# Performance work log

Measured on AMD Instinct MI355X. Metric: run time of the kernel, lower is better.

## Reference

```python
import jax, jax.numpy as jnp
import numpy as np
import math

D_IN, D_MODEL, N_HEADS, DIM_HEAD, NB_FEAT, N_CLASSES = 24, 512, 8, 64, 266, 10
FF_DIM = 4 * D_MODEL  # performer-pytorch FeedForward mult=4
LN_EPS = 1e-5
B, N = 16, 2048


def gaussian_orthogonal(key, nb_rows, nb_cols):
    # FAVOR+ gaussian orthogonal random matrix (scaling=0: chi-distributed row norms)
    n_blocks = nb_rows // nb_cols + 1
    keys = jax.random.split(key, n_blocks + 1)
    blocks = []
    for i in range(n_blocks):
        q, _ = jnp.linalg.qr(jax.random.normal(keys[i], (nb_cols, nb_cols)))
        blocks.append(q.T)
    mat = jnp.concatenate(blocks, axis=0)[:nb_rows]
    multiplier = jnp.linalg.norm(jax.random.normal(keys[-1], (nb_rows, nb_cols)), axis=1)
    return multiplier[:, None] * mat


def layer_norm(x, g, b):
    mu = jnp.mean(x, axis=-1, keepdims=True)
    var = jnp.var(x, axis=-1, keepdims=True)
    return (x - mu) * jax.lax.rsqrt(var + LN_EPS) * g + b


def softmax_kernel(data, proj, is_query, eps=1e-4):
    # FAVOR+ positive random features approximating the softmax kernel
    data_norm = data.shape[-1] ** -0.25
    ratio = proj.shape[0] ** -0.5
    dd = jnp.einsum('bhnd,fd->bhnf', data * data_norm, proj)  # [B,H,N,F]
    diag = 0.5 * jnp.sum(data * data, axis=-1, keepdims=True) * (data_norm ** 2)
    if is_query:
        m = jax.lax.stop_gradient(jnp.max(dd, axis=-1, keepdims=True))
    else:
        m = jax.lax.stop_gradient(jnp.max(dd))
    return ratio * (jnp.exp(dd - diag - m) + eps)


def setup_inputs() -> dict:
    key = jax.random.key(0)
    ks = jax.random.split(key, 24)

    def linw(k, fi, fo):
        bnd = 1.0 / math.sqrt(fi)
        return jax.random.uniform(k, (fi, fo), minval=-bnd, maxval=bnd, dtype=jnp.float32)

    def linb(k, fi, fo):
        bnd = 1.0 / math.sqrt(fi)
        return jax.random.uniform(k, (fo,), minval=-bnd, maxval=bnd, dtype=jnp.float32)

    return {
        'x': jax.random.normal(ks[0], (B, N, D_IN), dtype=jnp.float32),
        'enc_w': linw(ks[1], D_IN, D_MODEL), 'enc_b': linb(ks[2], D_IN, D_MODEL),
        'ln1_g': jnp.ones((D_MODEL,), jnp.float32), 'ln1_b': jnp.zeros((D_MODEL,), jnp.float32),
        'wq': linw(ks[3], D_MODEL, D_MODEL), 'bq': linb(ks[4], D_MODEL, D_MODEL),
        'wk': linw(ks[5], D_MODEL, D_MODEL), 'bk': linb(ks[6], D_MODEL, D_MODEL),
        'wv': linw(ks[7], D_MODEL, D_MODEL), 'bv': linb(ks[8], D_MODEL, D_MODEL),
        'wo': linw(ks[9], D_MODEL, D_MODEL), 'bo': linb(ks[10], D_MODEL, D_MODEL),
        'proj': gaussian_orthogonal(ks[11], NB_FEAT, DIM_HEAD).astype(jnp.float32),
        'ln2_g': jnp.ones((D_MODEL,), jnp.float32), 'ln2_b': jnp.zeros((D_MODEL,), jnp.float32),
        'ff_w1': linw(ks[12], D_MODEL, FF_DIM), 'ff_b1': linb(ks[13], D_MODEL, FF_DIM),
        'ff_w2': linw(ks[14], FF_DIM, D_MODEL), 'ff_b2': linb(ks[15], FF_DIM, D_MODEL),
        'mlp_w1': linw(ks[16], D_MODEL, D_MODEL), 'mlp_b1': linb(ks[17], D_MODEL, D_MODEL),
        'mlp_w2': linw(ks[18], D_MODEL, N_CLASSES), 'mlp_b2': linb(ks[19], D_MODEL, N_CLASSES),
    }


def reference(x, enc_w, enc_b, ln1_g, ln1_b, wq, bq, wk, bk, wv, bv, wo, bo, proj,
              ln2_g, ln2_b, ff_w1, ff_b1, ff_w2, ff_b2, mlp_w1, mlp_b1, mlp_w2, mlp_b2):
    b, n, _ = x.shape
    h = (x @ enc_w + enc_b) * math.sqrt(D_MODEL)  # [B,N,D]

    # --- Performer layer: PreLN + FAVOR+ self-attention ---
    y = layer_norm(h, ln1_g, ln1_b)
    split = lambda t: t.reshape(b, n, N_HEADS, DIM_HEAD).transpose(0, 2, 1, 3)  # [B,H,N,Dh]
    q = split(y @ wq + bq)
    k = split(y @ wk + bk)
    v = split(y @ wv + bv)
    qp = softmax_kernel(q, proj, is_query=True)   # [B,H,N,F]
    kp = softmax_kernel(k, proj, is_query=False)  # [B,H,N,F]
    # non-causal linear attention
    k_sum = kp.sum(axis=2)                                   # [B,H,F]
    d_inv = 1.0 / jnp.einsum('bhnf,bhf->bhn', qp, k_sum)     # [B,H,N]
    ctx = jnp.einsum('bhnf,bhnd->bhfd', kp, v)               # [B,H,F,Dh]
    attn = jnp.einsum('bhnf,bhfd,bhn->bhnd', qp, ctx, d_inv)
    attn = attn.transpose(0, 2, 1, 3).reshape(b, n, D_MODEL)
    h = h + attn @ wo + bo

    y = layer_norm(h, ln2_g, ln2_b)
    h = h + jax.nn.gelu(y @ ff_w1 + ff_b1, approximate=False) @ ff_w2 + ff_b2

    # --- max pool over sequence + MLP head ---
    p = jnp.max(h, axis=1)  # [B,D]
    return jax.nn.relu(p @ mlp_w1 + mlp_b1) @ mlp_w2 + mlp_b2  # [B,n_classes]
```

## Files before the change

### kernel.cpp

```cpp
#include <hip/hip_runtime.h>
#include <math.h>

typedef unsigned short u16;
typedef __bf16 bf16x8 __attribute__((ext_vector_type(8)));
typedef float f32x4 __attribute__((ext_vector_type(4)));
typedef u16 u16x8 __attribute__((ext_vector_type(8)));

#define DEVI static __device__ __forceinline__

#define NB 16
#define SEQ 2048
#define DM 512
#define DH 64
#define NF 266
#define NFP 288
#define FFD 2048
#define ROWS (NB*SEQ)
#define SQRT_DM 22.62741699796952f
#define DATA_NORM 0.3535533905932738f
#define RATIO 0.0613139073f
#define KEPS 1e-4f

DEVI u16 f2b(float f){
  union{float f; unsigned u;} c; c.f=f;
  unsigned r = c.u + 0x7FFFu + ((c.u>>16)&1u);
  return (u16)(r>>16);
}
DEVI float b2f(u16 v){
  union{unsigned u; float f;} c; c.u = ((unsigned)v)<<16; return c.f;
}
DEVI unsigned cvtpk(float a, float b){
  unsigned r;
  asm("v_cvt_pk_bf16_f32 %0, %1, %2" : "=v"(r) : "v"(a), "v"(b));
  return r;
}

DEVI f32x4 MFMA(bf16x8 a, bf16x8 b, f32x4 c){
  return __builtin_amdgcn_mfma_f32_16x16x32_bf16(a,b,c,0,0,0);
}

DEVI void async16(void* lds, const void* g){
  __builtin_amdgcn_global_load_lds(
      (const __attribute__((address_space(1))) unsigned*)g,
      (__attribute__((address_space(3))) unsigned*)lds, 16, 0, 0);
}

DEVI void atomicMaxF(float* a, float v){
  if (v >= 0.f) atomicMax((int*)a, __float_as_int(v));
  else          atomicMin((unsigned*)a, (unsigned)__float_as_int(v));
}

DEVI bf16x8 ldb8(const u16* p){ return *(const bf16x8*)p; }

DEVI float erf_fast(float u){
  float au = fabsf(u);
  float tt = __builtin_amdgcn_rcpf(1.f + 0.3275911f*au);
  float poly = tt*(0.254829592f + tt*(-0.284496736f + tt*(1.421413741f + tt*(-1.453152027f + tt*1.061405429f))));
  float er = 1.f - poly*__expf(-u*u);
  return copysignf(er, u);
}

template<int EPI, int BNT>
__launch_bounds__(512,2)
__global__ void gemm8(const u16* __restrict__ A, int lda,
                      const u16* __restrict__ Bt, int ldb,
                      const float* __restrict__ bias,
                      float* __restrict__ resid,
                      u16* __restrict__ Cb,
                      int N, int K)
{
  constexpr int NREG = BNT/64;
  constexpr int BUFU = 8192 + BNT*32;
  __shared__ u16 sm[2*BUFU];
  const int tid = threadIdx.x;
  const int ntn = N / BNT;
  int bid = blockIdx.x;
  const int nwg = gridDim.x;
  if ((nwg & 7) == 0){ int qq = nwg >> 3; bid = (bid & 7)*qq + (bid >> 3); }
  const int bm = bid / ntn, bn = bid % ntn;
  const int wid = tid>>6, l = tid&63, lr = l&15, lg = l>>4;
  const int wm = wid>>2, wn = wid&3;

  const int rA = tid>>2;
  const int cA = (tid&3) ^ ((rA>>1)&3);
  const u16* gA = A  + (size_t)(bm*256 + rA)*lda + cA*8;
  const u16* gB = Bt + (size_t)(bn*BNT + rA)*ldb + cA*8;
  const size_t stepA = (size_t)128*lda, stepB = (size_t)128*ldb;

  const int cc = ((lg ^ ((lr>>1)&3))<<3);
  const int aoff = (wm*128 + lr)*32 + cc;
  const int boff = 8192 + (wn*(BNT/4) + lr)*32 + cc;

  const int nt = K >> 5;
  f32x4 acc[8][NREG];
  #pragma unroll
  for (int m=0;m<8;m++)
    #pragma unroll
    for (int n=0;n<NREG;n++) acc[m][n]=(f32x4){0.f,0.f,0.f,0.f};

  {
    u16* sb = &sm[0];
    async16(&sb[tid*8],         gA);
    async16(&sb[4096 + tid*8],  gA + stepA);
    async16(&sb[8192 + tid*8],  gB);
    if (BNT == 256) async16(&sb[12288 + tid*8], gB + stepB);
  }
  asm volatile("s_waitcnt vmcnt(0)" ::: "memory");
  __builtin_amdgcn_s_barrier();
  __builtin_amdgcn_sched_barrier(0);

  for (int t=0; t<nt; ++t){
    if (t+1 < nt){
      u16* sb = &sm[((t+1)&1)*BUFU];
      const u16* a0 = gA + (t+1)*32;
      const u16* b0 = gB + (t+1)*32;
      async16(&sb[tid*8],         a0);
      async16(&sb[4096 + tid*8],  a0 + stepA);
      async16(&sb[8192 + tid*8],  b0);
      if (BNT == 256) async16(&sb[12288 + tid*8], b0 + stepB);
    }
    __builtin_amdgcn_sched_barrier(0);
    const u16* sb = &sm[(t&1)*BUFU];
    bf16x8 af[8], bfr[NREG];
    #pragma unroll
    for (int m=0;m<8;m++) af[m]  = ldb8(&sb[aoff + m*512]);
    #pragma unroll
    for (int n=0;n<NREG;n++) bfr[n] = ldb8(&sb[boff + n*512]);
    __builtin_amdgcn_s_setprio(1);
    #pragma unroll
    for (int m=0;m<8;m++)
      #pragma unroll
      for (int n=0;n<NREG;n++)
        acc[m][n] = MFMA(af[m], bfr[n], acc[m][n]);
    __builtin_amdgcn_s_setprio(0);
    if (t+1 < nt){
      asm volatile("s_waitcnt vmcnt(0)" ::: "memory");
      __builtin_amdgcn_s_barrier();
      __builtin_amdgcn_sched_barrier(0);
    }
  }

  if (EPI == 3){
    const int r0 = bm*256 + wm*128 + lg*4;
    const int c0 = bn*BNT + wn*(BNT/4) + lr;
    #pragma unroll
    for (int m=0;m<8;m++){
      #pragma unroll
      for (int n=0;n<NREG;n++){
        #pragma unroll
        for (int q=0;q<4;q++){
          int r = r0 + m*16 + q;
          int c = c0 + n*16;
          float v = acc[m][n][q] + bias[c];
          size_t idx = (size_t)r*N + c;
          resid[idx] = resid[idx] + v;
        }
      }
    }
  } else {
    __syncthreads();
    constexpr int OBW = (BNT==256) ? 72 : 40;
    constexpr int OWS = (BNT==256) ? 2336 : 1280;
    const int c0w = bn*BNT + wn*(BNT/4);
    const int r0m = bm*256 + wm*128;
    #pragma unroll
    for (int m=0;m<8;m++){
      u16* obw = &sm[wid*OWS + (m&1)*(OWS/2)];
      #pragma unroll
      for (int n=0;n<NREG;n++){
        #pragma unroll
        for (int q=0;q<4;q++){
          float v = acc[m][n][q] + bias[c0w + n*16 + lr];
          if (EPI==2) v = 0.5f*v*(1.f + erf_fast(v*0.70710678f));
          obw[(lg*4+q)*OBW + n*16 + lr] = f2b(v);
        }
      }
      asm volatile("s_waitcnt lgkmcnt(0)" ::: "memory");
      if (BNT == 256){
        int rowR = l>>3, ck = l&7;
        #pragma unroll
        for (int rr=0; rr<2; ++rr){
          int r2 = rowR + rr*8;
          uint4 v = *(const uint4*)&obw[r2*OBW + ck*8];
          *(uint4*)(Cb + (size_t)(r0m + m*16 + r2)*N + c0w + ck*8) = v;
        }
      } else {
        int rowR = l>>2, ck = l&3;
        uint4 v = *(const uint4*)&obw[rowR*OBW + ck*8];
        *(uint4*)(Cb + (size_t)(r0m + m*16 + rowR)*N + c0w + ck*8) = v;
      }
    }
  }
}

__launch_bounds__(256)
__global__ void k_prep(const float* __restrict__ wq, const float* __restrict__ wk,
                       const float* __restrict__ wv, const float* __restrict__ wo,
                       const float* __restrict__ ffw1, const float* __restrict__ ffw2,
                       const float* __restrict__ proj, const float* __restrict__ bk,
                       const float* __restrict__ bv,
                       u16* __restrict__ wqT, u16* __restrict__ wkvT, u16* __restrict__ woT,
                       u16* __restrict__ f1T, u16* __restrict__ f2T, u16* __restrict__ pjn,
                       float* __restrict__ kvb, float* __restrict__ pbuf)
{
  int bid = blockIdx.x, t = threadIdx.x;
  if (bid < 3072){
    const float* src; u16* dst; int R, C, tile;
    if      (bid < 256){ src=wq;  dst=wqT;          R=512; C=512;  tile=bid; }
    else if (bid < 512){ src=wk;  dst=wkvT;         R=512; C=512;  tile=bid-256; }
    else if (bid < 768){ src=wv;  dst=wkvT+262144;  R=512; C=512;  tile=bid-512; }
    else if (bid <1024){ src=wo;  dst=woT;          R=512; C=512;  tile=bid-768; }
    else if (bid <2048){ src=ffw1;dst=f1T;          R=512; C=2048; tile=bid-1024; }
    else               { src=ffw2;dst=f2T;          R=2048;C=512;  tile=bid-2048; }
    int ntc = C>>5;
    int tr = tile/ntc, tc = tile%ntc;
    __shared__ float tl[32][33];
    int r = t>>5, c = t&31;
    #pragma unroll
    for (int it=0; it<4; ++it)
      tl[r+it*8][c] = src[(size_t)(tr*32 + r + it*8)*C + tc*32 + c];
    __syncthreads();
    #pragma unroll
    for (int it=0; it<4; ++it)
      dst[(size_t)(tc*32 + r + it*8)*R + tr*32 + c] = f2b(tl[c][r+it*8]);
    return;
  }
  int i = (bid-3072)*256 + t;
  if (i < NFP*DH){ int f=i>>6, d=i&63; pjn[i] = f2b(f<NF ? proj[(size_t)f*64+d]*DATA_NORM : 0.f); return; }
  i -= NFP*DH;
  if (i < 1024){ kvb[i] = (i<512)? bk[i] : bv[i-512]; return; }
  i -= 1024;
  if (i < NB*DM){ pbuf[i] = -INFINITY; return; }
}

__global__ void k_signal(float* out, float v){
  if (threadIdx.x==0 && blockIdx.x==0) out[0] = v;
}

__launch_bounds__(256)
__global__ void k_encode_ln(const float* __restrict__ x, const float* __restrict__ ew,
                            const float* __restrict__ eb, const float* __restrict__ lgw,
                            const float* __restrict__ lbw, float* __restrict__ h,
                            u16* __restrict__ y)
{
  int w = threadIdx.x>>6, l = threadIdx.x&63;
  int row = blockIdx.x*4 + w;
  const float* xr = x + (size_t)row*24;
  float xv[24];
  #pragma unroll
  for (int k=0;k<24;k++) xv[k] = xr[k];
  int c0 = l*8;
  float a[8] = {0,0,0,0,0,0,0,0};
  #pragma unroll
  for (int k=0;k<24;k++){
    const float* wp = ew + (size_t)k*DM + c0;
    #pragma unroll
    for (int c=0;c<8;c++) a[c] += xv[k]*wp[c];
  }
  float s=0.f, s2=0.f;
  #pragma unroll
  for (int c=0;c<8;c++){
    a[c] = (a[c] + eb[c0+c]) * SQRT_DM;
    s += a[c]; s2 += a[c]*a[c];
  }
  #pragma unroll
  for (int m=1;m<64;m<<=1){ s += __shfl_xor(s,m); s2 += __shfl_xor(s2,m); }
  float mu = s*(1.f/DM);
  float rs = rsqrtf(s2*(1.f/DM) - mu*mu + 1e-5f);
  float* hr = h + (size_t)row*DM + c0;
  u16 yv[8];
  #pragma unroll
  for (int c=0;c<8;c++){
    hr[c] = a[c];
    yv[c] = f2b((a[c]-mu)*rs*lgw[c0+c] + lbw[c0+c]);
  }
  *(uint4*)(y + (size_t)row*DM + c0) = *(const uint4*)yv;
}

__launch_bounds__(256)
__global__ void k_ln(const float* __restrict__ h, const float* __restrict__ lgw,
                     const float* __restrict__ lbw, u16* __restrict__ y)
{
  int w = threadIdx.x>>6, l = threadIdx.x&63;
  int row = blockIdx.x*4 + w;
  int c0 = l*8;
  const float* hr = h + (size_t)row*DM + c0;
  float a[8];
  *(float4*)&a[0] = *(const float4*)hr;
  *(float4*)&a[4] = *(const float4*)(hr+4);
  float s=0.f, s2=0.f;
  #pragma unroll
  for (int c=0;c<8;c++){ s += a[c]; s2 += a[c]*a[c]; }
  #pragma unroll
  for (int m=1;m<64;m<<=1){ s += __shfl_xor(s,m); s2 += __shfl_xor(s2,m); }
  float mu = s*(1.f/DM);
  float rs = rsqrtf(s2*(1.f/DM) - mu*mu + 1e-5f);
  u16 yv[8];
  #pragma unroll
  for (int c=0;c<8;c++) yv[c] = f2b((a[c]-mu)*rs*lgw[c0+c] + lbw[c0+c]);
  *(uint4*)(y + (size_t)row*DM + c0) = *(const uint4*)yv;
}

__launch_bounds__(256,1)
__global__ void k_kmax(const u16* __restrict__ kv, const u16* __restrict__ pjn,
                       float* __restrict__ mkpart)
{
  __shared__ float red[4];
  int t = threadIdx.x, w = t>>6, l = t&63, lr = l&15, lg = l>>4;
  int bh = blockIdx.x>>3, tile = blockIdx.x&7;
  int b = bh>>3, hd = bh&7;
  int row0 = tile*256 + w*64;
  bf16x8 pf0[17], pf1[17];
  #pragma unroll
  for (int f=0; f<17; ++f){
    const u16* pb = pjn + (f*16 + lr)*64 + lg*8;
    pf0[f] = ldb8(pb); pf1[f] = ldb8(pb+32);
  }
  bf16x8 a0[4], a1[4];
  #pragma unroll
  for (int it=0; it<4; ++it){
    const u16* kb = kv + ((size_t)(b*SEQ + row0 + it*16 + lr)*1024 + hd*64 + lg*8);
    a0[it] = ldb8(kb); a1[it] = ldb8(kb+32);
  }
  float vmax = -3e38f;
  #pragma unroll
  for (int it=0; it<4; ++it){
    #pragma unroll
    for (int f=0; f<17; ++f){
      f32x4 z = (f32x4){0.f,0.f,0.f,0.f};
      z = MFMA(a0[it], pf0[f], z);
      z = MFMA(a1[it], pf1[f], z);
      if (f*16 + lr < NF){
        #pragma unroll
        for (int j=0;j<4;j++) vmax = fmaxf(vmax, z[j]);
      }
    }
  }
  #pragma unroll
  for (int m=1;m<64;m<<=1) vmax = fmaxf(vmax, __shfl_xor(vmax,m));
  if (l==0) red[w] = vmax;
  __syncthreads();
  if (t==0) mkpart[blockIdx.x] = fmaxf(fmaxf(red[0],red[1]), fmaxf(red[2],red[3]));
}

__global__ void k_kmax_red(const float* __restrict__ mkpart, float* __restrict__ mk){
  __shared__ float red[4];
  int t = threadIdx.x, w = t>>6, l = t&63;
  float v = fmaxf(fmaxf(mkpart[t], mkpart[t+256]), fmaxf(mkpart[t+512], mkpart[t+768]));
  #pragma unroll
  for (int m=1;m<64;m<<=1) v = fmaxf(v, __shfl_xor(v,m));
  if (l==0) red[w] = v;
  __syncthreads();
  if (t==0) mk[0] = fmaxf(fmaxf(red[0],red[1]), fmaxf(red[2],red[3]));
}

__launch_bounds__(256,2)
__global__ void k_kpctx(const u16* __restrict__ kv, const u16* __restrict__ pjn,
                        const float* __restrict__ mkp,
                        u16* __restrict__ ctxp, float* __restrict__ ksump)
{
  __shared__ u16 pjs[272*64];
  __shared__ u16 vT[DH*32];
  __shared__ u16 kpT[NFP*32];
  __shared__ float dbuf[4][16];
  int t = threadIdx.x, w = t>>6, l = t&63, lr = l&15, lg = l>>4;
  int bh = blockIdx.x>>2, seg = blockIdx.x&3;
  int b = bh>>3, hd = bh&7;
  int mw = w>>1, fh = (w&1)*9;
  float mk = *mkp;

  for (int i=t; i<2176; i+=256){
    int row = i>>3, cin = i&7;
    *(uint4*)&pjs[row*64 + ((cin ^ (row&7))<<3)] = ((const uint4*)pjn)[i];
  }

  f32x4 ctxa[18];
  #pragma unroll
  for (int f=0;f<18;f++) ctxa[f]=(f32x4){0.f,0.f,0.f,0.f};
  float ksa[9];
  #pragma unroll
  for (int i=0;i<9;i++) ksa[i]=0.f;

  for (int ch=0; ch<16; ++ch){
    int n0 = seg*512 + ch*32;
    __syncthreads();
    {
      int nl = t>>3, d0 = (t&7)*8;
      const u16* vsrc = kv + ((size_t)(b*SEQ + n0 + nl)*1024 + 512 + hd*64 + d0);
      uint4 vv = *(const uint4*)vsrc;
      const u16* vp = (const u16*)&vv;
      #pragma unroll
      for (int i=0;i<8;i++){
        int row = d0+i;
        vT[row*32 + (((nl>>3) ^ ((row>>1)&3))<<3) + (nl&7)] = vp[i];
      }
    }
    const u16* kb = kv + ((size_t)(b*SEQ + n0 + mw*16 + lr)*1024 + hd*64 + lg*8);
    bf16x8 a0 = ldb8(kb), a1 = ldb8(kb+32);
    float sq = 0.f;
    #pragma unroll
    for (int i=0;i<8;i++){ float u0=(float)a0[i], u1=(float)a1[i]; sq += u0*u0 + u1*u1; }
    sq += __shfl_xor(sq,16); sq += __shfl_xor(sq,32);
    if (l<16) dbuf[w][l] = sq*0.0625f;
    #pragma unroll
    for (int ff=0; ff<9; ++ff){
      int f = fh + ff;
      f32x4 z = (f32x4){0.f,0.f,0.f,0.f};
      if (f < 17){
        int row = f*16 + lr;
        const u16* pb0 = pjs + row*64 + ((lg ^ (lr&7))<<3);
        const u16* pb1 = pjs + row*64 + (((lg+4) ^ (lr&7))<<3);
        z = MFMA(a0, ldb8(pb0), z);
        z = MFMA(a1, ldb8(pb1), z);
      }
      float kp0 = RATIO*(__expf(z[0] - dbuf[w][lg*4+0] - mk) + KEPS);
      float kp1 = RATIO*(__expf(z[1] - dbuf[w][lg*4+1] - mk) + KEPS);
      float kp2 = RATIO*(__expf(z[2] - dbuf[w][lg*4+2] - mk) + KEPS);
      float kp3 = RATIO*(__expf(z[3] - dbuf[w][lg*4+3] - mk) + KEPS);
      ksa[ff] += kp0 + kp1 + kp2 + kp3;
      ushort4 kw;
      kw.x = f2b(kp0); kw.y = f2b(kp1); kw.z = f2b(kp2); kw.w = f2b(kp3);
      int row = f*16 + lr;
      int wch = (mw*2 + (lg>>1)) ^ ((row>>1)&3);
      *(ushort4*)&kpT[row*32 + (wch<<3) + ((lg&1)<<2)] = kw;
    }
    __syncthreads();
    int rr = w*16 + lr;
    bf16x8 av = ldb8(&vT[rr*32 + ((lg ^ ((rr>>1)&3))<<3)]);
    #pragma unroll
    for (int f=0;f<18;f++){
      int row = f*16 + lr;
      ctxa[f] = MFMA(av, ldb8(&kpT[row*32 + ((lg ^ ((row>>1)&3))<<3)]), ctxa[f]);
    }
  }

  __syncthreads();
  {
    float* tb = (w&1) ? (float*)pjs : (float*)kpT;
    u16* dstq = ctxp + (((size_t)seg*128 + bh)*DH + w*16)*NFP;
    #pragma unroll
    for (int r=0; r<2; ++r){
      if ((w>>1) == r){
        #pragma unroll
        for (int f=0;f<18;f++)
          #pragma unroll
          for (int j=0;j<4;j++)
            tb[(lg*4+j)*NFP + f*16 + lr] = ctxa[f][j];
        asm volatile("s_waitcnt lgkmcnt(0)" ::: "memory");
        #pragma unroll
        for (int k=0;k<9;k++){
          int c = k*64 + l;
          f32x4 v0 = *(const f32x4*)(tb + c*8);
          f32x4 v1 = *(const f32x4*)(tb + c*8 + 4);
          u16x8 o;
          o[0]=f2b(v0[0]); o[1]=f2b(v0[1]); o[2]=f2b(v0[2]); o[3]=f2b(v0[3]);
          o[4]=f2b(v1[0]); o[5]=f2b(v1[1]); o[6]=f2b(v1[2]); o[7]=f2b(v1[3]);
          *(u16x8*)(dstq + c*8) = o;
        }
      }
      __syncthreads();
    }
  }
  #pragma unroll
  for (int ff=0;ff<9;ff++){
    float v = ksa[ff];
    v += __shfl_xor(v,16); v += __shfl_xor(v,32);
    if (l<16) ksump[((size_t)seg*128 + bh)*NFP + (fh+ff)*16 + l] = v;
  }
}

__global__ void k_reduce(const u16* __restrict__ ctxp, const float* __restrict__ ksump,
                         u16* __restrict__ ctxb, float* __restrict__ ksum)
{
  const size_t CT = (size_t)128*DH*NFP;
  const size_t KT = (size_t)128*NFP;
  size_t i = (size_t)blockIdx.x*256 + threadIdx.x;
  if (i < CT){
    float s = b2f(ctxp[i]) + b2f(ctxp[i+CT]) + b2f(ctxp[i+2*CT]) + b2f(ctxp[i+3*CT]);
    ctxb[i] = f2b(s);
  } else if (i < CT + KT){
    size_t j = i - CT;
    ksum[j] = ksump[j] + ksump[j+KT] + ksump[j+2*KT] + ksump[j+3*KT];
  }
}

__launch_bounds__(256,3)
__global__ void k_qp_attn(const u16* __restrict__ q, const u16* __restrict__ pjn,
                          const u16* __restrict__ ctxb, const float* __restrict__ ksum,
                          u16* __restrict__ attn)
{
  __shared__ u16 pjs[272*64];
  __shared__ u16 ob[4][16*72];
  int t = threadIdx.x, w = t>>6, l = t&63, lr = l&15, lg = l>>4;
  int bh = blockIdx.x>>5, tile = blockIdx.x&31;
  int b = bh>>3, hd = bh&7;
  int n0 = tile*64;

  for (int i=t; i<2176; i+=256){
    int row = i>>3, cin = i&7;
    *(uint4*)&pjs[row*64 + ((cin ^ (row&7))<<3)] = ((const uint4*)pjn)[i];
  }

  const u16* qb = q + ((size_t)(b*SEQ + n0 + w*16 + lr)*DM + hd*64 + lg*8);
  bf16x8 a0 = ldb8(qb), a1 = ldb8(qb+32);
  float sq = 0.f;
  #pragma unroll
  for (int i=0;i<8;i++){ float u0=(float)a0[i], u1=(float)a1[i]; sq += u0*u0 + u1*u1; }
  sq += __shfl_xor(sq,16); sq += __shfl_xor(sq,32);
  float dg = sq*0.0625f;

  __syncthreads();

  const int sw0 = ((lg ^ (lr&7))<<3);
  const int sw1 = (((lg+4) ^ (lr&7))<<3);

  float mj = -3e38f;
  #pragma unroll
  for (int ft=0; ft<17; ++ft){
    const u16* pb = pjs + (ft*16 + lr)*64;
    f32x4 z = (f32x4){0.f,0.f,0.f,0.f};
    z = MFMA(ldb8(pb + sw0), a0, z);
    z = MFMA(ldb8(pb + sw1), a1, z);
    if (ft < 16){
      #pragma unroll
      for (int j=0;j<4;j++) mj = fmaxf(mj, z[j]);
    } else {
      #pragma unroll
      for (int j=0;j<4;j++) if (lg*4+j < 10) mj = fmaxf(mj, z[j]);
    }
  }
  mj = fmaxf(mj, __shfl_xor(mj,16));
  mj = fmaxf(mj, __shfl_xor(mj,32));

  int s0 = ((lg&1)<<5) + lr;
  int s1 = s0 + 16;
  bool hi = (l >= 32);
  f32x4 oacc[4];
  #pragma unroll
  for (int d=0;d<4;d++) oacc[d]=(f32x4){0.f,0.f,0.f,0.f};
  const u16* cbase = ctxb + (size_t)bh*DH*NFP;
  const float* ksb = ksum + (size_t)bh*NFP;
  float den = 0.f;
  #pragma unroll
  for (int fp=0; fp<9; ++fp){
    int te = 2*fp, to = te+1;
    f32x4 z0 = (f32x4){0.f,0.f,0.f,0.f};
    f32x4 z1 = (f32x4){0.f,0.f,0.f,0.f};
    {
      const u16* pb = pjs + (te*16 + lr)*64;
      z0 = MFMA(ldb8(pb + sw0), a0, z0);
      z0 = MFMA(ldb8(pb + sw1), a1, z0);
    }
    if (to < 17){
      const u16* pb = pjs + (to*16 + lr)*64;
      z1 = MFMA(ldb8(pb + sw0), a0, z1);
      z1 = MFMA(ldb8(pb + sw1), a1, z1);
    }
    f32x4 ks0 = *(const f32x4*)(ksb + te*16 + lg*4);
    f32x4 ks1 = *(const f32x4*)(ksb + to*16 + lg*4);
    int fb0 = te*16 + lg*4, fb1 = to*16 + lg*4;
    float qv0[4], qv1[4];
    #pragma unroll
    for (int j=0;j<4;j++){
      qv0[j] = (fb0 + j < NF) ? RATIO*(__expf(z0[j] - dg - mj) + KEPS) : 0.f;
      den += qv0[j]*ks0[j];
      qv1[j] = (fb1 + j < NF) ? RATIO*(__expf(z1[j] - dg - mj) + KEPS) : 0.f;
      den += qv1[j]*ks1[j];
    }
    unsigned q00 = cvtpk(qv0[0], qv0[1]), q01 = cvtpk(qv0[2], qv0[3]);
    unsigned q10 = cvtpk(qv1[0], qv1[1]), q11 = cvtpk(qv1[2], qv1[3]);
    unsigned e0 = (unsigned)__shfl((int)q00, s0), o0 = (unsigned)__shfl((int)q10, s0);
    unsigned e1 = (unsigned)__shfl((int)q01, s0), o1 = (unsigned)__shfl((int)q11, s0);
    unsigned e2 = (unsigned)__shfl((int)q00, s1), o2 = (unsigned)__shfl((int)q10, s1);
    unsigned e3 = (unsigned)__shfl((int)q01, s1), o3 = (unsigned)__shfl((int)q11, s1);
    union { unsigned u[4]; bf16x8 v; } bw;
    bw.u[0] = hi ? o0 : e0;
    bw.u[1] = hi ? o1 : e1;
    bw.u[2] = hi ? o2 : e2;
    bw.u[3] = hi ? o3 : e3;
    #pragma unroll
    for (int d=0;d<4;d++)
      oacc[d] = MFMA(bw.v, ldb8(&cbase[(d*16 + lr)*NFP + fp*32 + lg*8]), oacc[d]);
  }
  den += __shfl_xor(den,16); den += __shfl_xor(den,32);
  float di = 1.f/den;
  float di4[4];
  #pragma unroll
  for (int j=0;j<4;j++) di4[j] = __shfl(di, lg*4+j);

  u16* obw = ob[w];
  #pragma unroll
  for (int d=0;d<4;d++)
    #pragma unroll
    for (int j=0;j<4;j++)
      obw[(lg*4+j)*72 + d*16 + lr] = f2b(oacc[d][j]*di4[j]);
  asm volatile("s_waitcnt lgkmcnt(0)" ::: "memory");
  {
    int row = l>>3, ck = l&7;
    #pragma unroll
    for (int rr=0; rr<2; ++rr){
      int r2 = row + rr*8;
      uint4 v = *(const uint4*)&obw[r2*72 + ck*8];
      u16* ab = attn + ((size_t)(b*SEQ + n0 + w*16 + r2))*DM + hd*64;
      *(uint4*)(ab + ck*8) = v;
    }
  }
}

__global__ void k_maxpool(const float* __restrict__ h, const u16* __restrict__ fo,
                          float* __restrict__ p){
  int bi = blockIdx.x;
  int b = bi>>5, half = (bi>>4)&1, seg = bi&15;
  int c = half*256 + threadIdx.x;
  size_t base = ((size_t)b*SEQ + seg*128)*DM + c;
  const float* hp = h + base;
  const u16*  fp = fo + base;
  float m = -3e38f;
  for (int n=0;n<128;n++) m = fmaxf(m, hp[(size_t)n*DM] + b2f(fp[(size_t)n*DM]));
  atomicMaxF(&p[b*DM + c], m);
}

__launch_bounds__(256)
__global__ void k_head(const float* __restrict__ p, const float* __restrict__ w1,
                       const float* __restrict__ b1, const float* __restrict__ w2,
                       const float* __restrict__ b2, float* __restrict__ out)
{
  __shared__ float z[DM];
  __shared__ float pr[DM];
  int b = blockIdx.x, t = threadIdx.x;
  pr[t] = p[(size_t)b*DM + t];
  pr[t+256] = p[(size_t)b*DM + t + 256];
  __syncthreads();
  for (int c=t; c<DM; c+=256){
    float a = b1[c];
    for (int k=0;k<DM;k++) a += pr[k]*w1[(size_t)k*DM + c];
    z[c] = fmaxf(a, 0.f);
  }
  __syncthreads();
  if (t < 10){
    float a = b2[t];
    for (int k=0;k<DM;k++) a += z[k]*w2[(size_t)k*10 + t];
    out[b*10 + t] = a;
  }
}

static inline size_t align256(size_t x){ return (x+255)&~(size_t)255; }

extern "C" void kernel_launch(void* const* d_in, const int* in_sizes, int n_in,
                              void* d_out, int out_size, void* d_ws, size_t ws_size,
                              hipStream_t stream)
{
  (void)in_sizes; (void)n_in; (void)out_size;
  const float* x     = (const float*)d_in[0];
  const float* enc_w = (const float*)d_in[1];
  const float* enc_b = (const float*)d_in[2];
  const float* ln1_g = (const float*)d_in[3];
  const float* ln1_b = (const float*)d_in[4];
  const float* wq    = (const float*)d_in[5];
  const float* bq    = (const float*)d_in[6];
  const float* wk    = (const float*)d_in[7];
  const float* bk    = (const float*)d_in[8];
  const float* wv    = (const float*)d_in[9];
  const float* bv    = (const float*)d_in[10];
  const float* wo    = (const float*)d_in[11];
  const float* bo    = (const float*)d_in[12];
  const float* proj  = (const float*)d_in[13];
  const float* ln2_g = (const float*)d_in[14];
  const float* ln2_b = (const float*)d_in[15];
  const float* ff_w1 = (const float*)d_in[16];
  const float* ff_b1 = (const float*)d_in[17];
  const float* ff_w2 = (const float*)d_in[18];
  const float* ff_b2 = (const float*)d_in[19];
  const float* mw1   = (const float*)d_in[20];
  const float* mb1   = (const float*)d_in[21];
  const float* mw2   = (const float*)d_in[22];
  const float* mb2   = (const float*)d_in[23];

  char* base = (char*)d_ws;
  size_t off = 0;
  auto alloc = [&](size_t bytes)->void*{ void* r = base + off; off = align256(off + bytes); return r; };
  float* h     = (float*)alloc((size_t)ROWS*DM*4);
  u16*   slotA = (u16*)  alloc((size_t)ROWS*DM*2);
  u16*   wqT   = (u16*)  alloc((size_t)512*512*2);
  u16*   wkvT  = (u16*)  alloc((size_t)1024*512*2);
  u16*   woT   = (u16*)  alloc((size_t)512*512*2);
  u16*   f1T   = (u16*)  alloc((size_t)2048*512*2);
  u16*   f2T   = (u16*)  alloc((size_t)512*2048*2);
  u16*   pjn   = (u16*)  alloc((size_t)NFP*DH*2);
  float* kvb   = (float*)alloc(1024*4);
  float* mk    = (float*)alloc(256);
  float* mkpart= (float*)alloc(1024*4);
  u16*   ctxb  = (u16*)  alloc((size_t)128*DH*NFP*2);
  float* ksum  = (float*)alloc((size_t)128*NFP*4);
  float* pbuf  = (float*)alloc((size_t)NB*DM*4);
  size_t offU = off;
  u16*   slotB = (u16*)  alloc((size_t)ROWS*1024*2);
  u16*   ctxp  = (u16*)  alloc((size_t)4*128*DH*NFP*2);
  float* ksump = (float*)alloc((size_t)4*128*NFP*4);
  size_t off_small = off;
  size_t off_big   = align256(offU + (size_t)ROWS*FFD*2);
  bool big = (off_big <= ws_size);
  u16* ffb = (u16*)(base + offU);
  if (off_small > ws_size){
    k_signal<<<1,64,0,stream>>>((float*)d_out, (float)ws_size);
    return;
  }

  u16* y    = slotA;
  u16* attn = slotA;
  u16* ffo  = slotA;
  u16* kvB  = slotB;
  u16* qB   = slotB;

  k_prep<<<3180,256,0,stream>>>(wq, wk, wv, wo, ff_w1, ff_w2, proj, bk, bv,
                                wqT, wkvT, woT, f1T, f2T, pjn, kvb, pbuf);

  k_encode_ln<<<ROWS/4,256,0,stream>>>(x, enc_w, enc_b, ln1_g, ln1_b, h, y);
  gemm8<1,256><<<(ROWS/256)*(1024/256),512,0,stream>>>(y,512, wkvT,512, kvb, nullptr, kvB, 1024, 512);
  k_kmax<<<1024,256,0,stream>>>(kvB, pjn, mkpart);
  k_kmax_red<<<1,256,0,stream>>>(mkpart, mk);
  k_kpctx<<<512,256,0,stream>>>(kvB, pjn, mk, ctxp, ksump);
  k_reduce<<<9360,256,0,stream>>>(ctxp, ksump, ctxb, ksum);
  gemm8<1,128><<<(ROWS/256)*(512/128),512,0,stream>>>(y,512, wqT,512, bq, nullptr, qB, 512, 512);
  k_qp_attn<<<128*32,256,0,stream>>>(qB, pjn, ctxb, ksum, attn);
  gemm8<3,128><<<(ROWS/256)*(512/128),512,0,stream>>>(attn,512, woT,512, bo, h, nullptr, 512, 512);
  k_ln<<<ROWS/4,256,0,stream>>>(h, ln2_g, ln2_b, y);
  if (big){
    gemm8<2,256><<<(ROWS/256)*(2048/256),512,0,stream>>>(y,512, f1T,512, ff_b1, nullptr, ffb, 2048, 512);
    gemm8<1,128><<<(ROWS/256)*(512/128),512,0,stream>>>(ffb,2048, f2T,2048, ff_b2, nullptr, ffo, 512, 2048);
  } else {
    for (int c2=0;c2<2;c2++){
      const u16* ych = y + (size_t)c2*16384*512;
      u16*       fch = ffo + (size_t)c2*16384*512;
      gemm8<2,256><<<(16384/256)*(2048/256),512,0,stream>>>(ych,512, f1T,512, ff_b1, nullptr, ffb, 2048, 512);
      gemm8<1,128><<<(16384/256)*(512/128),512,0,stream>>>(ffb,2048, f2T,2048, ff_b2, nullptr, fch, 512, 2048);
    }
  }
  k_maxpool<<<NB*32,256,0,stream>>>(h, ffo, pbuf);
  k_head<<<NB,256,0,stream>>>(pbuf, mw1, mb1, mw2, mb2, (float*)d_out);
}
```

Baseline: 606.0 us.

## Triple-buffer GEMM LDS with prefetch distance two and split MFMA phases

Moves the bf16 GEMM from double to triple buffering in LDS, issuing global-to-LDS loads two K-steps ahead and waiting with partial vmcnt instead of draining all loads. Each K-step is split into two halves, each interleaving A or B prefetch with LDS reads and MFMAs, with extra barriers between them. The goal is to hide global memory latency better and overlap LDS reads with MFMA work. The cost is 1.5x the LDS footprint, which can cut occupancy at launch bounds of 2 blocks per CU, plus additional barriers per iteration.

```diff
diff --git a/kernel.cpp b/kernel.cpp
--- a/kernel.cpp
+++ b/kernel.cpp
@@ -70,8 +70,8 @@
                       int N, int K)
 {
   constexpr int NREG = BNT/64;
-  constexpr int BUFU = 8192 + BNT*32;
-  __shared__ u16 sm[2*BUFU];
+  constexpr int LDSB = 8192 + BNT*32;
+  __shared__ u16 sm[3*LDSB];
   const int tid = threadIdx.x;
   const int ntn = N / BNT;
   int bid = blockIdx.x;
@@ -98,46 +98,83 @@
     #pragma unroll
     for (int n=0;n<NREG;n++) acc[m][n]=(f32x4){0.f,0.f,0.f,0.f};
 
-  {
-    u16* sb = &sm[0];
-    async16(&sb[tid*8],         gA);
-    async16(&sb[4096 + tid*8],  gA + stepA);
-    async16(&sb[8192 + tid*8],  gB);
-    if (BNT == 256) async16(&sb[12288 + tid*8], gB + stepB);
-  }
-  asm volatile("s_waitcnt vmcnt(0)" ::: "memory");
+  auto stageA = [&](int bufi, int t){
+    u16* sb = &sm[bufi*LDSB];
+    const u16* a0 = gA + t*32;
+    async16(&sb[tid*8],        a0);
+    async16(&sb[4096 + tid*8], a0 + stepA);
+  };
+  auto stageB = [&](int bufi, int t){
+    u16* sb = &sm[bufi*LDSB];
+    const u16* b0 = gB + t*32;
+    async16(&sb[8192 + tid*8], b0);
+    if (BNT == 256) async16(&sb[12288 + tid*8], b0 + stepB);
+  };
+
+  stageA(0,0); stageB(0,0);
+  stageA(1,1); stageB(1,1);
+  if constexpr (BNT == 256) asm volatile("s_waitcnt vmcnt(4)" ::: "memory");
+  else                      asm volatile("s_waitcnt vmcnt(3)" ::: "memory");
   __builtin_amdgcn_s_barrier();
   __builtin_amdgcn_sched_barrier(0);
 
+  int bufc = 0;
   for (int t=0; t<nt; ++t){
+    const u16* sb = &sm[bufc*LDSB];
+    int bufn = bufc+2; if (bufn>=3) bufn-=3;
+    const bool pre = (t+2 < nt);
+    bf16x8 bfr[NREG];
+
+    if (pre) stageA(bufn, t+2);
+    bf16x8 af0 = ldb8(&sb[aoff + 0*512]);
+    bf16x8 af1 = ldb8(&sb[aoff + 1*512]);
+    bf16x8 af2 = ldb8(&sb[aoff + 2*512]);
+    bf16x8 af3 = ldb8(&sb[aoff + 3*512]);
+    #pragma unroll
+    for (int n=0;n<NREG;n++) bfr[n] = ldb8(&sb[boff + n*512]);
+    __builtin_amdgcn_s_barrier();
+    asm volatile("s_waitcnt lgkmcnt(0)" ::: "memory");
+    __builtin_amdgcn_sched_barrier(0);
+    __builtin_amdgcn_s_setprio(1);
+    #pragma unroll
+    for (int n=0;n<NREG;n++){
+      acc[0][n] = MFMA(af0, bfr[n], acc[0][n]);
+      acc[1][n] = MFMA(af1, bfr[n], acc[1][n]);
+      acc[2][n] = MFMA(af2, bfr[n], acc[2][n]);
+      acc[3][n] = MFMA(af3, bfr[n], acc[3][n]);
+    }
+    __builtin_amdgcn_s_setprio(0);
+    __builtin_amdgcn_s_barrier();
+
+    if (pre) stageB(bufn, t+2);
+    bf16x8 af4 = ldb8(&sb[aoff + 4*512]);
+    bf16x8 af5 = ldb8(&sb[aoff + 5*512]);
+    bf16x8 af6 = ldb8(&sb[aoff + 6*512]);
+    bf16x8 af7 = ldb8(&sb[aoff + 7*512]);
+    __builtin_amdgcn_s_barrier();
+    asm volatile("s_waitcnt lgkmcnt(0)" ::: "memory");
+    __builtin_amdgcn_sched_barrier(0);
+    __builtin_amdgcn_s_setprio(1);
+    #pragma unroll
+    for (int n=0;n<NREG;n++){
+      acc[4][n] = MFMA(af4, bfr[n], acc[4][n]);
+      acc[5][n] = MFMA(af5, bfr[n], acc[5][n]);
+      acc[6][n] = MFMA(af6, bfr[n], acc[6][n]);
+      acc[7][n] = MFMA(af7, bfr[n], acc[7][n]);
+    }
+    __builtin_amdgcn_s_setprio(0);
+
     if (t+1 < nt){
-      u16* sb = &sm[((t+1)&1)*BUFU];
-      const u16* a0 = gA + (t+1)*32;
-      const u16* b0 = gB + (t+1)*32;
-      async16(&sb[tid*8],         a0);
-      async16(&sb[4096 + tid*8],  a0 + stepA);
-      async16(&sb[8192 + tid*8],  b0);
-      if (BNT == 256) async16(&sb[12288 + tid*8], b0 + stepB);
-    }
-    __builtin_amdgcn_sched_barrier(0);
-    const u16* sb = &sm[(t&1)*BUFU];
-    bf16x8 af[8], bfr[NREG];
-    #pragma unroll
-    for (int m=0;m<8;m++) af[m]  = ldb8(&sb[aoff + m*512]);
-    #pragma unroll
-    for (int n=0;n<NREG;n++) bfr[n] = ldb8(&sb[boff + n*512]);
-    __builtin_amdgcn_s_setprio(1);
-    #pragma unroll
-    for (int m=0;m<8;m++)
-      #pragma unroll
-      for (int n=0;n<NREG;n++)
-        acc[m][n] = MFMA(af[m], bfr[n], acc[m][n]);
-    __builtin_amdgcn_s_setprio(0);
-    if (t+1 < nt){
-      asm volatile("s_waitcnt vmcnt(0)" ::: "memory");
+      if (pre){
+        if constexpr (BNT == 256) asm volatile("s_waitcnt vmcnt(4)" ::: "memory");
+        else                      asm volatile("s_waitcnt vmcnt(3)" ::: "memory");
+      } else {
+        asm volatile("s_waitcnt vmcnt(0)" ::: "memory");
+      }
       __builtin_amdgcn_s_barrier();
       __builtin_amdgcn_sched_barrier(0);
     }
+    bufc = bufc+1; if (bufc>=3) bufc-=3;
   }
 
   if (EPI == 3){
```

After: 620.2 us. 1.02x slower.
